# Optimization experiments

Hardware: AMD Instinct MI355X
Metric: run time of the kernel (lower is better)

Reference implementation:

```python
import jax, jax.numpy as jnp
import numpy as np

B, S, D, H, L = 8, 1024, 512, 8, 6
DK = D // H
DFF = 4 * D
EPS = 1e-5
SCALE = float(np.sqrt(DK))  # torch: sqrt(d_k)


def setup_inputs() -> dict:
    key = jax.random.key(0)
    ks = jax.random.split(key, 10)
    init = lambda k, shape: jax.random.normal(k, shape, jnp.float32) * 0.02
    return {
        "x": jax.random.normal(ks[0], (B, S, D), jnp.float32),
        "qkv_w": init(ks[1], (L, D, 3 * D)),
        "qkv_b": init(ks[2], (L, 3 * D)),
        "out_w": init(ks[3], (L, D, D)),
        "out_b": init(ks[4], (L, D)),
        "ln1_g": jnp.ones((L, D), jnp.float32),
        "ln1_b": jnp.zeros((L, D), jnp.float32),
        "mlp_w1": init(ks[5], (L, D, DFF)),
        "mlp_b1": init(ks[6], (L, DFF)),
        "mlp_w2": init(ks[7], (L, DFF, D)),
        "mlp_b2": init(ks[8], (L, D)),
        "ln2_g": jnp.ones((L, D), jnp.float32),
        "ln2_b": jnp.zeros((L, D), jnp.float32),
    }


def _layer_norm(x, g, b):
    m = jnp.mean(x, axis=-1, keepdims=True)
    v = jnp.var(x, axis=-1, keepdims=True)  # biased var, matches torch LayerNorm
    return (x - m) * jax.lax.rsqrt(v + EPS) * g + b


def reference(x, qkv_w, qkv_b, out_w, out_b, ln1_g, ln1_b,
              mlp_w1, mlp_b1, mlp_w2, mlp_b2, ln2_g, ln2_b):
    b, s, d = x.shape
    causal = jnp.tril(jnp.ones((s, s), dtype=bool))  # [S,S]
    for i in range(L):
        # --- causal self-attention, post-LN residual (dropout = eval identity) ---
        qkv = x @ qkv_w[i] + qkv_b[i]                      # [B,S,3D]
        q, k, v = jnp.split(qkv, 3, axis=-1)
        q = q.reshape(b, s, H, DK)
        k = k.reshape(b, s, H, DK)
        v = v.reshape(b, s, H, DK)
        att = jnp.einsum('bqhd,bkhd->bhqk', q, k) / SCALE  # [B,H,S,S]
        att = jnp.where(causal, att, -jnp.inf)
        att = jax.nn.softmax(att, axis=-1)
        o = jnp.einsum('bhqk,bkhd->bqhd', att, v).reshape(b, s, d)
        x = _layer_norm(o @ out_w[i] + out_b[i] + x, ln1_g[i], ln1_b[i])
        # --- MLP, post-LN residual ---
        h = jax.nn.relu(x @ mlp_w1[i] + mlp_b1[i]) @ mlp_w2[i] + mlp_b2[i]
        x = _layer_norm(x + h, ln2_g[i], ln2_b[i])
    return x
```

## Files before the change

kernel.cpp:

```cpp
#include <hip/hip_runtime.h>
#include <math.h>

#define Bn   8
#define Sn   1024
#define Dn   512
#define Hn   8
#define DKn  64
#define Ln   6
#define DFFn 2048
#define Mn   (Bn * Sn)

typedef __bf16 bf16x8 __attribute__((ext_vector_type(8)));
typedef __bf16 bf16x4 __attribute__((ext_vector_type(4)));
typedef __bf16 bf16x2 __attribute__((ext_vector_type(2)));
typedef float  f32x4  __attribute__((ext_vector_type(4)));

__device__ __forceinline__ void gl_lds16(const void* g, void* l) {
    __builtin_amdgcn_global_load_lds(
        (const __attribute__((address_space(1))) void*)g,
        (__attribute__((address_space(3))) void*)l, 16, 0, 0);
}

__global__ __launch_bounds__(256) void k_cast_bf16(const float* __restrict__ in,
                                                   __bf16* __restrict__ out, int n) {
    int i = blockIdx.x * 256 + threadIdx.x;
    if (i < n) out[i] = (__bf16)in[i];
}

__global__ __launch_bounds__(256) void k_trans_all(
    const float* __restrict__ qkv_w, const float* __restrict__ out_w,
    const float* __restrict__ w1, const float* __restrict__ w2,
    __bf16* __restrict__ Wq, __bf16* __restrict__ Wo,
    __bf16* __restrict__ W1o, __bf16* __restrict__ W2o)
{
    const int lay = blockIdx.x / 3072;
    const int t   = blockIdx.x % 3072;
    const float* src; __bf16* dst; int K, N, n0, k0;
    if (t < 768)       { src = qkv_w + (size_t)lay * Dn * 3 * Dn; dst = Wq  + (size_t)lay * 3 * Dn * Dn;
                         K = 512;  N = 1536; int u = t;        n0 = (u % 48) * 32; k0 = (u / 48) * 32; }
    else if (t < 1024) { src = out_w + (size_t)lay * Dn * Dn;     dst = Wo  + (size_t)lay * Dn * Dn;
                         K = 512;  N = 512;  int u = t - 768;  n0 = (u % 16) * 32; k0 = (u / 16) * 32; }
    else if (t < 2048) { src = w1 + (size_t)lay * Dn * DFFn;      dst = W1o + (size_t)lay * DFFn * Dn;
                         K = 512;  N = 2048; int u = t - 1024; n0 = (u % 64) * 32; k0 = (u / 64) * 32; }
    else               { src = w2 + (size_t)lay * DFFn * Dn;      dst = W2o + (size_t)lay * Dn * DFFn;
                         K = 2048; N = 512;  int u = t - 2048; n0 = (u % 16) * 32; k0 = (u / 16) * 32; }

    __shared__ float tt[32][33];
    const int tx = threadIdx.x, ty = threadIdx.y;
    #pragma unroll
    for (int r = 0; r < 4; r++)
        tt[ty + 8 * r][tx] = src[(size_t)(k0 + ty + 8 * r) * N + n0 + tx];
    __syncthreads();
    #pragma unroll
    for (int r = 0; r < 4; r++)
        dst[(size_t)(n0 + ty + 8 * r) * K + k0 + tx] = (__bf16)tt[tx][ty + 8 * r];
}

template <int RELU, int OUTBF, int JT, int VW, int BK>
__global__ __launch_bounds__(256) void k_gemm_mfma(
    const __bf16* __restrict__ A, const __bf16* __restrict__ Bt,
    const float* __restrict__ bias, void* __restrict__ Cout,
    __bf16* __restrict__ Vt, int M, int N, int K, int NBX)
{
    constexpr int BN = JT * 32;
    constexpr int UR = BK / 8;
    constexpr int HC = BK / 32;
    __shared__ __bf16 As[128][BK];
    __shared__ __bf16 Bs[BN][BK];
    const int tid  = threadIdx.x;
    const int lane = tid & 63;
    const int wave = tid >> 6;
    const int wy   = wave >> 1, wx = wave & 1;
    const int m16  = lane & 15, quad = lane >> 4;

    const int cpx = gridDim.x >> 3;
    const int id  = (blockIdx.x & 7) * cpx + (blockIdx.x >> 3);
    const int bm  = (id / NBX) * 128;
    const int bn  = (id % NBX) * BN;

    f32x4 acc[4][JT];
    #pragma unroll
    for (int i = 0; i < 4; i++)
        #pragma unroll
        for (int j = 0; j < JT; j++)
            acc[i][j] = (f32x4){0.f, 0.f, 0.f, 0.f};

    const __bf16* Ap = A  + (size_t)bm * K;
    const __bf16* Bp = Bt + (size_t)bn * K;

    int sw[HC];
    #pragma unroll
    for (int hc = 0; hc < HC; hc++)
        sw[hc] = ((quad + 4 * hc) ^ (m16 & (UR - 1))) * 8;

    for (int k0 = 0; k0 < K; k0 += BK) {
        __syncthreads();
        #pragma unroll
        for (int c = 0; c < UR / 2; c++) {
            int lin = tid + c * 256;
            int row = lin / UR, uu = lin % UR;
            int su  = (uu ^ (row & (UR - 1))) << 3;
            gl_lds16(Ap + (size_t)row * K + k0 + su, (void*)(&As[0][0] + lin * 8));
        }
        #pragma unroll
        for (int c = 0; c < (JT * UR) / 8; c++) {
            int lin = tid + c * 256;
            int row = lin / UR, uu = lin % UR;
            int su  = (uu ^ (row & (UR - 1))) << 3;
            gl_lds16(Bp + (size_t)row * K + k0 + su, (void*)(&Bs[0][0] + lin * 8));
        }
        __syncthreads();

        bf16x8 af[4][HC], bfr[JT][HC];
        #pragma unroll
        for (int i = 0; i < 4; i++)
            #pragma unroll
            for (int hc = 0; hc < HC; hc++)
                af[i][hc] = *(const bf16x8*)&As[wy * 64 + i * 16 + m16][sw[hc]];
        #pragma unroll
        for (int j = 0; j < JT; j++)
            #pragma unroll
            for (int hc = 0; hc < HC; hc++)
                bfr[j][hc] = *(const bf16x8*)&Bs[wx * JT * 16 + j * 16 + m16][sw[hc]];
        #pragma unroll
        for (int hc = 0; hc < HC; hc++)
            #pragma unroll
            for (int i = 0; i < 4; i++)
                #pragma unroll
                for (int j = 0; j < JT; j++)
                    acc[i][j] = __builtin_amdgcn_mfma_f32_16x16x32_bf16(
                        af[i][hc], bfr[j][hc], acc[i][j], 0, 0, 0);
    }

    float*  Cf = (float*)Cout;
    __bf16* Cb = (__bf16*)Cout;
    #pragma unroll
    for (int i = 0; i < 4; i++) {
        const int row0 = bm + wy * 64 + i * 16 + quad * 4;
        #pragma unroll
        for (int j = 0; j < JT; j++) {
            const int col = bn + wx * JT * 16 + j * 16 + m16;
            const float bv = bias[col];
            float vv[4];
            #pragma unroll
            for (int r = 0; r < 4; r++) {
                float v = acc[i][j][r] + bv;
                if (RELU) v = fmaxf(v, 0.f);
                vv[r] = v;
                if (OUTBF) Cb[(size_t)(row0 + r) * N + col] = (__bf16)v;
                else       Cf[(size_t)(row0 + r) * N + col] = v;
            }
            if (VW && col >= 1024) {
                const int cc = col - 1024;
                const int bb = row0 >> 10, ss = row0 & 1023;
                bf16x4 pv;
                #pragma unroll
                for (int r = 0; r < 4; r++) pv[r] = (__bf16)vv[r];
                *(bf16x4*)&Vt[((size_t)(bb * Hn + (cc >> 6)) * DKn + (cc & 63)) * Sn + ss] = pv;
            }
        }
    }
}

__device__ __forceinline__ void softmax_update(
    f32x4 sv[4], float m[4], float l[4], f32x4 acc[4],
    bool diag, int wave16, int quad, int m16,
    __bf16 (*Pw)[72], bf16x8& pf0, bf16x8& pf1)
{
    #pragma unroll
    for (int j = 0; j < 4; j++)
        #pragma unroll
        for (int r = 0; r < 4; r++) {
            float v = sv[j][r] * 0.125f;
            if (diag && (j * 16 + m16) > (wave16 + quad * 4 + r)) v = -1e30f;
            sv[j][r] = v;
        }

    float pm[4];
    #pragma unroll
    for (int r = 0; r < 4; r++)
        pm[r] = fmaxf(fmaxf(sv[0][r], sv[1][r]), fmaxf(sv[2][r], sv[3][r]));
    #pragma unroll
    for (int off = 1; off < 16; off <<= 1)
        #pragma unroll
        for (int r = 0; r < 4; r++)
            pm[r] = fmaxf(pm[r], __shfl_xor(pm[r], off, 16));

    bool grew = false;
    #pragma unroll
    for (int r = 0; r < 4; r++) grew = grew || (pm[r] > m[r] + 8.f);
    if (__any((int)grew)) {
        #pragma unroll
        for (int r = 0; r < 4; r++) {
            float mn = fmaxf(m[r], pm[r]);
            float al = __expf(m[r] - mn);
            m[r] = mn;
            l[r] *= al;
            #pragma unroll
            for (int j = 0; j < 4; j++) acc[j][r] *= al;
        }
    }

    float rs[4] = {0.f, 0.f, 0.f, 0.f};
    #pragma unroll
    for (int j = 0; j < 4; j++)
        #pragma unroll
        for (int r = 0; r < 4; r++) {
            float p = __expf(sv[j][r] - m[r]);
            rs[r] += p;
            Pw[quad * 4 + r][j * 16 + m16] = (__bf16)p;
        }
    #pragma unroll
    for (int off = 1; off < 16; off <<= 1)
        #pragma unroll
        for (int r = 0; r < 4; r++)
            rs[r] += __shfl_xor(rs[r], off, 16);
    #pragma unroll
    for (int r = 0; r < 4; r++) l[r] += rs[r];

    pf0 = *(const bf16x8*)&Pw[m16][quad * 8];
    pf1 = *(const bf16x8*)&Pw[m16][32 + quad * 8];
}

__global__ __launch_bounds__(256, 3) void k_attn_mfma(
    const __bf16* __restrict__ qkv, const __bf16* __restrict__ Vt,
    __bf16* __restrict__ o)
{
    const int id = blockIdx.x;
    const int h  = id & 7;
    const int b  = (id >> 3) & 7;
    const int qt = id >> 6;
    const int tid  = threadIdx.x;
    const int lane = tid & 63, wave = tid >> 6;
    const int m16  = lane & 15, quad = lane >> 4;
    const int wave16 = wave * 16;

    __shared__ __bf16 Kb[2][64][64];
    __shared__ __bf16 Vb[2][64][64];
    __shared__ __bf16 Ps[4][16][72];

    const __bf16* base = qkv + (size_t)b * Sn * 1536 + h * DKn;
    const __bf16* vtb  = Vt + (size_t)(b * Hn + h) * DKn * Sn;
    __bf16 (*Pw)[72] = Ps[wave];

    const int sw0 = ((quad    ) ^ (m16 & 7)) * 8;
    const int sw1 = ((quad + 4) ^ (m16 & 7)) * 8;

    #define STAGE(KT, BB)                                                       \
        {                                                                       \
            _Pragma("unroll")                                                   \
            for (int c = 0; c < 2; c++) {                                       \
                const int lin = tid + c * 256;                                  \
                const int row = lin >> 3, uu = lin & 7;                         \
                const int su  = (uu ^ (row & 7)) * 8;                           \
                gl_lds16(base + (size_t)((KT) * 64 + row) * 1536 + 512 + su,    \
                         (void*)(&Kb[BB][0][0] + lin * 8));                     \
                gl_lds16(vtb + (size_t)row * Sn + (KT) * 64 + su,               \
                         (void*)(&Vb[BB][0][0] + lin * 8));                     \
            }                                                                   \
        }

    STAGE(0, 0);

    bf16x8 q0, q1;
    {
        const __bf16* qa = base + (size_t)(qt * 64 + wave16 + m16) * 1536 + quad * 8;
        q0 = *(const bf16x8*)qa; q1 = *(const bf16x8*)(qa + 32);
    }

    float m[4], l[4];
    f32x4 acc[4];
    #pragma unroll
    for (int r = 0; r < 4; r++) {
        m[r] = -1e30f; l[r] = 0.f;
        acc[r] = (f32x4){0.f, 0.f, 0.f, 0.f};
    }

    __syncthreads();

    for (int kt = 0; kt <= qt; kt++) {
        const int buf = kt & 1;
        if (kt < qt) STAGE(kt + 1, buf ^ 1);

        f32x4 sv[4];
        __builtin_amdgcn_s_setprio(1);
        #pragma unroll
        for (int j = 0; j < 4; j++) {
            const int rk = j * 16 + m16;
            bf16x8 kf0 = *(const bf16x8*)&Kb[buf][rk][sw0];
            bf16x8 kf1 = *(const bf16x8*)&Kb[buf][rk][sw1];
            f32x4 s = (f32x4){0.f, 0.f, 0.f, 0.f};
            s = __builtin_amdgcn_mfma_f32_16x16x32_bf16(q0, kf0, s, 0, 0, 0);
            s = __builtin_amdgcn_mfma_f32_16x16x32_bf16(q1, kf1, s, 0, 0, 0);
            sv[j] = s;
        }
        __builtin_amdgcn_s_setprio(0);

        bf16x8 vf[4][2];
        #pragma unroll
        for (int jd = 0; jd < 4; jd++) {
            const int rv = jd * 16 + m16;
            vf[jd][0] = *(const bf16x8*)&Vb[buf][rv][sw0];
            vf[jd][1] = *(const bf16x8*)&Vb[buf][rv][sw1];
        }

        bf16x8 p0, p1;
        softmax_update(sv, m, l, acc, kt == qt, wave16, quad, m16, Pw, p0, p1);

        __builtin_amdgcn_s_setprio(1);
        #pragma unroll
        for (int jd = 0; jd < 4; jd++) {
            acc[jd] = __builtin_amdgcn_mfma_f32_16x16x32_bf16(p0, vf[jd][0], acc[jd], 0, 0, 0);
            acc[jd] = __builtin_amdgcn_mfma_f32_16x16x32_bf16(p1, vf[jd][1], acc[jd], 0, 0, 0);
        }
        __builtin_amdgcn_s_setprio(0);

        __syncthreads();
    }
    #undef STAGE

    #pragma unroll
    for (int r = 0; r < 4; r++) l[r] = 1.0f / l[r];
    #pragma unroll
    for (int jd = 0; jd < 4; jd++)
        #pragma unroll
        for (int r = 0; r < 4; r++) {
            const int row = b * Sn + qt * 64 + wave16 + quad * 4 + r;
            o[(size_t)row * Dn + h * DKn + jd * 16 + m16] = (__bf16)(acc[jd][r] * l[r]);
        }
}

template <int FINAL>
__global__ __launch_bounds__(256) void k_residual_ln(
    const __bf16* __restrict__ t, __bf16* __restrict__ xb,
    const float* __restrict__ g, const float* __restrict__ be,
    float* __restrict__ outf)
{
    const int row  = (blockIdx.x << 2) | (threadIdx.x >> 6);
    const int lane = threadIdx.x & 63;
    const size_t base = (size_t)row * Dn + lane * 8;

    bf16x8 tv = *(const bf16x8*)&t[base];
    bf16x8 xv = *(const bf16x8*)&xb[base];
    float v[8];
    float s = 0.f;
    #pragma unroll
    for (int i = 0; i < 8; i++) {
        v[i] = (float)tv[i] + (float)xv[i];
        s += v[i];
    }
    #pragma unroll
    for (int off = 1; off < 64; off <<= 1) s += __shfl_xor(s, off);
    const float mean = s * (1.0f / Dn);

    float vs = 0.f;
    #pragma unroll
    for (int i = 0; i < 8; i++) {
        v[i] -= mean;
        vs += v[i] * v[i];
    }
    #pragma unroll
    for (int off = 1; off < 64; off <<= 1) vs += __shfl_xor(vs, off);
    const float inv = rsqrtf(vs * (1.0f / Dn) + 1e-5f);

    const f32x4 g0 = *(const f32x4*)&g[lane * 8];
    const f32x4 g1 = *(const f32x4*)&g[lane * 8 + 4];
    const f32x4 b0 = *(const f32x4*)&be[lane * 8];
    const f32x4 b1 = *(const f32x4*)&be[lane * 8 + 4];

    if (FINAL) {
        f32x4 o0, o1;
        #pragma unroll
        for (int i = 0; i < 4; i++) {
            o0[i] = v[i] * inv * g0[i] + b0[i];
            o1[i] = v[i + 4] * inv * g1[i] + b1[i];
        }
        *(f32x4*)&outf[base]     = o0;
        *(f32x4*)&outf[base + 4] = o1;
    } else {
        bf16x8 ov;
        #pragma unroll
        for (int i = 0; i < 4; i++) {
            ov[i]     = (__bf16)(v[i] * inv * g0[i] + b0[i]);
            ov[i + 4] = (__bf16)(v[i + 4] * inv * g1[i] + b1[i]);
        }
        *(bf16x8*)&xb[base] = ov;
    }
}

extern "C" void kernel_launch(void* const* d_in, const int* in_sizes, int n_in,
                              void* d_out, int out_size, void* d_ws, size_t ws_size,
                              hipStream_t stream)
{
    const float* x_in   = (const float*)d_in[0];
    const float* qkv_w  = (const float*)d_in[1];
    const float* qkv_b  = (const float*)d_in[2];
    const float* out_w  = (const float*)d_in[3];
    const float* out_b  = (const float*)d_in[4];
    const float* ln1_g  = (const float*)d_in[5];
    const float* ln1_b  = (const float*)d_in[6];
    const float* mlp_w1 = (const float*)d_in[7];
    const float* mlp_b1 = (const float*)d_in[8];
    const float* mlp_w2 = (const float*)d_in[9];
    const float* mlp_b2 = (const float*)d_in[10];
    const float* ln2_g  = (const float*)d_in[11];
    const float* ln2_b  = (const float*)d_in[12];

    char* p = (char*)d_ws;
    __bf16* Xb    = (__bf16*)p; p += (size_t)Mn * Dn * 2;
    __bf16* QKVb  = (__bf16*)p; p += (size_t)Mn * 3 * Dn * 2;
    __bf16* AOb   = (__bf16*)p; p += (size_t)Mn * Dn * 2;
    __bf16* Hb    = (__bf16*)p; p += (size_t)Mn * DFFn * 2;
    __bf16* BUF3b = (__bf16*)p; p += (size_t)Mn * Dn * 2;
    __bf16* Wq    = (__bf16*)p; p += (size_t)Ln * 3 * Dn * Dn * 2;
    __bf16* Wo    = (__bf16*)p; p += (size_t)Ln * Dn * Dn * 2;
    __bf16* W1    = (__bf16*)p; p += (size_t)Ln * DFFn * Dn * 2;
    __bf16* W2    = (__bf16*)p; p += (size_t)Ln * Dn * DFFn * 2;
    __bf16* Vt    = Hb;

    k_cast_bf16<<<(Mn * Dn) / 256, 256, 0, stream>>>(x_in, Xb, Mn * Dn);

    k_trans_all<<<Ln * 3072, dim3(32, 8), 0, stream>>>(
        qkv_w, out_w, mlp_w1, mlp_w2, Wq, Wo, W1, W2);

    for (int l = 0; l < Ln; l++) {
        const __bf16* Wql = Wq + (size_t)l * 3 * Dn * Dn;
        const __bf16* Wol = Wo + (size_t)l * Dn * Dn;
        const __bf16* W1l = W1 + (size_t)l * DFFn * Dn;
        const __bf16* W2l = W2 + (size_t)l * Dn * DFFn;

        k_gemm_mfma<0, 1, 4, 1, 64><<<768, 256, 0, stream>>>(
            Xb, Wql, qkv_b + (size_t)l * 3 * Dn, QKVb, Vt, Mn, 3 * Dn, Dn, 12);
        k_attn_mfma<<<1024, 256, 0, stream>>>(QKVb, Vt, AOb);
        k_gemm_mfma<0, 1, 2, 0, 128><<<512, 256, 0, stream>>>(
            AOb, Wol, out_b + (size_t)l * Dn, BUF3b, nullptr, Mn, Dn, Dn, 8);
        k_residual_ln<0><<<Mn / 4, 256, 0, stream>>>(BUF3b, Xb,
            ln1_g + (size_t)l * Dn, ln1_b + (size_t)l * Dn, nullptr);
        k_gemm_mfma<1, 1, 4, 0, 64><<<1024, 256, 0, stream>>>(
            Xb, W1l, mlp_b1 + (size_t)l * DFFn, Hb, nullptr, Mn, DFFn, Dn, 16);
        k_gemm_mfma<0, 1, 2, 0, 128><<<512, 256, 0, stream>>>(
            Hb, W2l, mlp_b2 + (size_t)l * Dn, BUF3b, nullptr, Mn, Dn, DFFn, 8);
        if (l == Ln - 1)
            k_residual_ln<1><<<Mn / 4, 256, 0, stream>>>(BUF3b, Xb,
                ln2_g + (size_t)l * Dn, ln2_b + (size_t)l * Dn, (float*)d_out);
        else
            k_residual_ln<0><<<Mn / 4, 256, 0, stream>>>(BUF3b, Xb,
                ln2_g + (size_t)l * Dn, ln2_b + (size_t)l * Dn, nullptr);
    }
}
```

Measured before the change: 956.1 us.

## Pair complementary causal query tiles per 512-thread attention block to share K/V

Each attention block now runs 8 waves covering two query tiles, qt and 15-qt. This balances the causal workload across blocks and lets both tiles share every staged K/V tile, so each block does the same total work and K/V global traffic per query tile drops. Staging is one 16-byte load per thread, with explicit vmcnt/lgkmcnt waits and raw barriers in place of __syncthreads. The cost is that the waves holding the shorter tile sit idle at the barriers for the remaining iterations, and the larger blocks may change occupancy.

```diff
diff --git a/kernel.cpp b/kernel.cpp
--- a/kernel.cpp
+++ b/kernel.cpp
@@ -222,22 +222,26 @@
     pf1 = *(const bf16x8*)&Pw[m16][32 + quad * 8];
 }
 
-__global__ __launch_bounds__(256, 3) void k_attn_mfma(
+__global__ __launch_bounds__(512, 4) void k_attn_mfma(
     const __bf16* __restrict__ qkv, const __bf16* __restrict__ Vt,
     __bf16* __restrict__ o)
 {
     const int id = blockIdx.x;
+    const int u  = id >> 6;
+    const int pr = (u < 4) ? u : 11 - u;
+    const int b  = (id >> 3) & 7;
     const int h  = id & 7;
-    const int b  = (id >> 3) & 7;
-    const int qt = id >> 6;
     const int tid  = threadIdx.x;
     const int lane = tid & 63, wave = tid >> 6;
     const int m16  = lane & 15, quad = lane >> 4;
-    const int wave16 = wave * 16;
+    const int isB  = wave >> 2;
+    const int wave16 = (wave & 3) * 16;
+    const int qtA  = pr, qtB = 15 - pr;
+    const int qt   = isB ? qtB : qtA;
 
     __shared__ __bf16 Kb[2][64][64];
     __shared__ __bf16 Vb[2][64][64];
-    __shared__ __bf16 Ps[4][16][72];
+    __shared__ __bf16 Ps[8][16][72];
 
     const __bf16* base = qkv + (size_t)b * Sn * 1536 + h * DKn;
     const __bf16* vtb  = Vt + (size_t)(b * Hn + h) * DKn * Sn;
@@ -246,18 +250,15 @@
     const int sw0 = ((quad    ) ^ (m16 & 7)) * 8;
     const int sw1 = ((quad + 4) ^ (m16 & 7)) * 8;
 
+    const int srow = tid >> 3;
+    const int ssu  = ((tid & 7) ^ (srow & 7)) * 8;
+
     #define STAGE(KT, BB)                                                       \
         {                                                                       \
-            _Pragma("unroll")                                                   \
-            for (int c = 0; c < 2; c++) {                                       \
-                const int lin = tid + c * 256;                                  \
-                const int row = lin >> 3, uu = lin & 7;                         \
-                const int su  = (uu ^ (row & 7)) * 8;                           \
-                gl_lds16(base + (size_t)((KT) * 64 + row) * 1536 + 512 + su,    \
-                         (void*)(&Kb[BB][0][0] + lin * 8));                     \
-                gl_lds16(vtb + (size_t)row * Sn + (KT) * 64 + su,               \
-                         (void*)(&Vb[BB][0][0] + lin * 8));                     \
-            }                                                                   \
+            gl_lds16(base + (size_t)((KT) * 64 + srow) * 1536 + 512 + ssu,      \
+                     (void*)(&Kb[BB][0][0] + tid * 8));                         \
+            gl_lds16(vtb + (size_t)srow * Sn + (KT) * 64 + ssu,                 \
+                     (void*)(&Vb[BB][0][0] + tid * 8));                         \
         }
 
     STAGE(0, 0);
@@ -276,46 +277,53 @@
         acc[r] = (f32x4){0.f, 0.f, 0.f, 0.f};
     }
 
-    __syncthreads();
-
-    for (int kt = 0; kt <= qt; kt++) {
+    for (int kt = 0; kt <= qtB; kt++) {
         const int buf = kt & 1;
-        if (kt < qt) STAGE(kt + 1, buf ^ 1);
-
-        f32x4 sv[4];
-        __builtin_amdgcn_s_setprio(1);
-        #pragma unroll
-        for (int j = 0; j < 4; j++) {
-            const int rk = j * 16 + m16;
-            bf16x8 kf0 = *(const bf16x8*)&Kb[buf][rk][sw0];
-            bf16x8 kf1 = *(const bf16x8*)&Kb[buf][rk][sw1];
-            f32x4 s = (f32x4){0.f, 0.f, 0.f, 0.f};
-            s = __builtin_amdgcn_mfma_f32_16x16x32_bf16(q0, kf0, s, 0, 0, 0);
-            s = __builtin_amdgcn_mfma_f32_16x16x32_bf16(q1, kf1, s, 0, 0, 0);
-            sv[j] = s;
-        }
-        __builtin_amdgcn_s_setprio(0);
-
-        bf16x8 vf[4][2];
-        #pragma unroll
-        for (int jd = 0; jd < 4; jd++) {
-            const int rv = jd * 16 + m16;
-            vf[jd][0] = *(const bf16x8*)&Vb[buf][rv][sw0];
-            vf[jd][1] = *(const bf16x8*)&Vb[buf][rv][sw1];
-        }
-
-        bf16x8 p0, p1;
-        softmax_update(sv, m, l, acc, kt == qt, wave16, quad, m16, Pw, p0, p1);
-
-        __builtin_amdgcn_s_setprio(1);
-        #pragma unroll
-        for (int jd = 0; jd < 4; jd++) {
-            acc[jd] = __builtin_amdgcn_mfma_f32_16x16x32_bf16(p0, vf[jd][0], acc[jd], 0, 0, 0);
-            acc[jd] = __builtin_amdgcn_mfma_f32_16x16x32_bf16(p1, vf[jd][1], acc[jd], 0, 0, 0);
-        }
-        __builtin_amdgcn_s_setprio(0);
-
-        __syncthreads();
+        if (kt < qtB) {
+            STAGE(kt + 1, buf ^ 1);
+            asm volatile("s_waitcnt vmcnt(2)" ::: "memory");
+        } else {
+            asm volatile("s_waitcnt vmcnt(0)" ::: "memory");
+        }
+        __builtin_amdgcn_s_barrier();
+
+        if (isB || kt <= qtA) {
+            f32x4 sv[4];
+            __builtin_amdgcn_s_setprio(1);
+            #pragma unroll
+            for (int j = 0; j < 4; j++) {
+                const int rk = j * 16 + m16;
+                bf16x8 kf0 = *(const bf16x8*)&Kb[buf][rk][sw0];
+                bf16x8 kf1 = *(const bf16x8*)&Kb[buf][rk][sw1];
+                f32x4 s = (f32x4){0.f, 0.f, 0.f, 0.f};
+                s = __builtin_amdgcn_mfma_f32_16x16x32_bf16(q0, kf0, s, 0, 0, 0);
+                s = __builtin_amdgcn_mfma_f32_16x16x32_bf16(q1, kf1, s, 0, 0, 0);
+                sv[j] = s;
+            }
+            __builtin_amdgcn_s_setprio(0);
+
+            bf16x8 vf[4][2];
+            #pragma unroll
+            for (int jd = 0; jd < 4; jd++) {
+                const int rv = jd * 16 + m16;
+                vf[jd][0] = *(const bf16x8*)&Vb[buf][rv][sw0];
+                vf[jd][1] = *(const bf16x8*)&Vb[buf][rv][sw1];
+            }
+
+            bf16x8 p0, p1;
+            softmax_update(sv, m, l, acc, kt == qt, wave16, quad, m16, Pw, p0, p1);
+
+            __builtin_amdgcn_s_setprio(1);
+            #pragma unroll
+            for (int jd = 0; jd < 4; jd++) {
+                acc[jd] = __builtin_amdgcn_mfma_f32_16x16x32_bf16(p0, vf[jd][0], acc[jd], 0, 0, 0);
+                acc[jd] = __builtin_amdgcn_mfma_f32_16x16x32_bf16(p1, vf[jd][1], acc[jd], 0, 0, 0);
+            }
+            __builtin_amdgcn_s_setprio(0);
+        }
+
+        asm volatile("s_waitcnt lgkmcnt(0)" ::: "memory");
+        __builtin_amdgcn_s_barrier();
     }
     #undef STAGE
 
@@ -431,7 +439,7 @@
 
         k_gemm_mfma<0, 1, 4, 1, 64><<<768, 256, 0, stream>>>(
             Xb, Wql, qkv_b + (size_t)l * 3 * Dn, QKVb, Vt, Mn, 3 * Dn, Dn, 12);
-        k_attn_mfma<<<1024, 256, 0, stream>>>(QKVb, Vt, AOb);
+        k_attn_mfma<<<512, 512, 0, stream>>>(QKVb, Vt, AOb);
         k_gemm_mfma<0, 1, 2, 0, 128><<<512, 256, 0, stream>>>(
             AOb, Wol, out_b + (size_t)l * Dn, BUF3b, nullptr, Mn, Dn, Dn, 8);
         k_residual_ln<0><<<Mn / 4, 256, 0, stream>>>(BUF3b, Xb,
```

After: 951.6 us. About the same (-0.5%).
